# Kernel optimization log

Hardware: AMD Instinct MI355X
Metric: run time of the kernel (lower is better)

The kernel has to match this reference:

```python
import jax, jax.numpy as jnp
import numpy as np

B, S, D_MODEL, HEADS, DK = 2, 2048, 1024, 16, 64


def setup_inputs() -> dict:
    key = jax.random.key(0)
    ks = jax.random.split(key, 7)
    scale = 0.02
    return {
        "query": jax.random.normal(ks[0], (B, S, D_MODEL), jnp.float32),
        "key": jax.random.normal(ks[1], (B, S, D_MODEL), jnp.float32),
        "value": jax.random.normal(ks[2], (B, S, D_MODEL), jnp.float32),
        "Wq": jax.random.normal(ks[3], (D_MODEL, HEADS * DK), jnp.float32) * scale,
        "bq": jax.random.normal(ks[4], (HEADS * DK,), jnp.float32) * scale,
        "Wo": jax.random.normal(ks[5], (HEADS * DK, D_MODEL), jnp.float32) * scale,
        "bo": jax.random.normal(ks[6], (D_MODEL,), jnp.float32) * scale,
    }


def reference(query, key, value, Wq, bq, Wo, bo):
    # NOTE: faithful to the original code, which (buggily) uses _W_q to
    # project query, key AND value, and scales by sqrt(seq_len), not sqrt(d_k).
    seq_len = key.shape[1]

    def split_heads(x):
        # [B,S,H*DK] -> [H,B,S,DK]; torch chunk(dim=-1)+cat(dim=0) stacks head h
        # (slice h*DK:(h+1)*DK) at batch block h.
        p = x @ Wq + bq
        b, s, _ = p.shape
        return p.reshape(b, s, HEADS, DK).transpose(2, 0, 1, 3)

    q = split_heads(query)   # [H,B,S,DK]
    k = split_heads(key)
    v = split_heads(value)

    inv_scale = jnp.float32(1.0 / np.sqrt(seq_len))
    scores = jnp.einsum("hbqd,hbkd->hbqk", q, k) * inv_scale  # [H,B,S,S]
    attn = jax.nn.softmax(scores, axis=-1)
    out = jnp.einsum("hbqk,hbkd->hbqd", attn, v)  # [H,B,S,DK]
    # inverse of chunk(dim=0)+cat(dim=-1): [H,B,S,DK] -> [B,S,H*DK]
    out = out.transpose(1, 2, 0, 3).reshape(query.shape[0], query.shape[1], HEADS * DK)
    return out @ Wo + bo
```

## Files before the change

kernel.cpp:

```cpp
#include <hip/hip_runtime.h>

#define DEVI __device__ __forceinline__

typedef short short4_t __attribute__((ext_vector_type(4)));
typedef short short8_t __attribute__((ext_vector_type(8)));
typedef __bf16 bf16x8 __attribute__((ext_vector_type(8)));
typedef float f32x4 __attribute__((ext_vector_type(4)));

DEVI short f2bf(float f) {
    union { float f; unsigned u; } v; v.f = f;
    unsigned r = (v.u + 0x7fffu + ((v.u >> 16) & 1u)) >> 16;
    return (short)r;
}

DEVI unsigned pack_ru(float a, float b) {
    union { float f; unsigned u; } x, y; x.f = a; y.f = b;
    return __builtin_amdgcn_perm(y.u + 0x8000u, x.u + 0x8000u, 0x07060302u);
}

DEVI void g2lds16(const short* g, short* l) {
    __builtin_amdgcn_global_load_lds(
        (const __attribute__((address_space(1))) void*)g,
        (__attribute__((address_space(3))) void*)l, 16, 0, 0);
}

__global__ __launch_bounds__(256) void prep_kernel(const float* __restrict__ q,
                                                   const float* __restrict__ k,
                                                   const float* __restrict__ v,
                                                   short* __restrict__ X,
                                                   const float* __restrict__ Wq,
                                                   short* __restrict__ WqT,
                                                   const float* __restrict__ Wo,
                                                   short* __restrict__ WoT) {
    __shared__ short T[64][65];
    const int bx = blockIdx.x;
    const int t = threadIdx.x;
    if (bx < 12288) {
        const size_t N1 = (size_t)4096 * 1024;
        size_t e = ((size_t)bx * 256 + t) * 4;
        const float* src; size_t off;
        if (e < N1)            { src = q; off = e; }
        else if (e < 2 * N1)   { src = k; off = e - N1; }
        else                   { src = v; off = e - 2 * N1; }
        f32x4 f = *(const f32x4*)(src + off);
        short4_t o;
        o[0] = f2bf(f[0]); o[1] = f2bf(f[1]); o[2] = f2bf(f[2]); o[3] = f2bf(f[3]);
        *(short4_t*)(X + e) = o;
        return;
    }
    const int which = bx - 12288;
    const float* W = (which < 256) ? Wq : Wo;
    short* Wt      = (which < 256) ? WqT : WoT;
    const int bxx = which & 255;
    const int kt = (bxx & 15) * 64, nt = (bxx >> 4) * 64;
#pragma unroll
    for (int r = 0; r < 4; ++r) {
        int kl = (t >> 4) + 16 * r;
        int n0 = (t & 15) * 4;
        f32x4 f = *(const f32x4*)(W + (size_t)(kt + kl) * 1024 + nt + n0);
#pragma unroll
        for (int j = 0; j < 4; ++j) T[n0 + j][kl] = f2bf(f[j]);
    }
    __syncthreads();
#pragma unroll
    for (int r = 0; r < 2; ++r) {
        int nl = (t >> 3) + 32 * r;
        int k0 = (t & 7) * 8;
        short8_t vv;
#pragma unroll
        for (int j = 0; j < 8; ++j) vv[j] = T[nl][k0 + j];
        *(short8_t*)(Wt + (size_t)(nt + nl) * 1024 + kt + k0) = vv;
    }
}

template <typename OutT>
__global__ __launch_bounds__(256) void gemm_bt_kernel(const short* __restrict__ A,
                                                      const short* __restrict__ Bt,
                                                      const float* __restrict__ bias,
                                                      OutT* __restrict__ C,
                                                      int M, int N, int K,
                                                      int qrows, float qscale) {
    __shared__ __align__(16) short As[2][128 * 32];
    __shared__ __align__(16) short Bs[2][128 * 32];
    const int tid  = threadIdx.x;
    const int lane = tid & 63, wave = tid >> 6;
    const int quad = lane >> 4, l16 = lane & 15;
    const int row0 = blockIdx.x * 128, col0 = blockIdx.y * 128;
    const int wm = (wave >> 1) * 64, wn = (wave & 1) * 64;
    const int srow = lane >> 2;
    const int scol = (lane & 3) * 8;
    f32x4 acc[4][4] = {};
#pragma unroll
    for (int r = 0; r < 2; ++r) {
        int rb = r * 64 + wave * 16;
        g2lds16(A  + (size_t)(row0 + rb + srow) * K + scol, &As[0][rb * 32]);
        g2lds16(Bt + (size_t)(col0 + rb + srow) * K + scol, &Bs[0][rb * 32]);
    }
    __syncthreads();
    int buf = 0;
    for (int k0 = 0; k0 < K; k0 += 32) {
        if (k0 + 32 < K) {
#pragma unroll
            for (int r = 0; r < 2; ++r) {
                int rb = r * 64 + wave * 16;
                g2lds16(A  + (size_t)(row0 + rb + srow) * K + k0 + 32 + scol, &As[buf ^ 1][rb * 32]);
                g2lds16(Bt + (size_t)(col0 + rb + srow) * K + k0 + 32 + scol, &Bs[buf ^ 1][rb * 32]);
            }
        }
        bf16x8 af[4], bfr[4];
#pragma unroll
        for (int mi = 0; mi < 4; ++mi) af[mi]  = *(const bf16x8*)&As[buf][(wm + mi * 16 + l16) * 32 + quad * 8];
#pragma unroll
        for (int ni = 0; ni < 4; ++ni) bfr[ni] = *(const bf16x8*)&Bs[buf][(wn + ni * 16 + l16) * 32 + quad * 8];
#pragma unroll
        for (int mi = 0; mi < 4; ++mi)
#pragma unroll
            for (int ni = 0; ni < 4; ++ni)
                acc[mi][ni] = __builtin_amdgcn_mfma_f32_16x16x32_bf16(af[mi], bfr[ni], acc[mi][ni], 0, 0, 0);
        __syncthreads();
        buf ^= 1;
    }
#pragma unroll
    for (int mi = 0; mi < 4; ++mi) {
#pragma unroll
        for (int ni = 0; ni < 4; ++ni) {
            int col = col0 + wn + ni * 16 + l16;
            float bv = bias[col];
#pragma unroll
            for (int i = 0; i < 4; ++i) {
                int row = row0 + wm + mi * 16 + quad * 4 + i;
                float val = acc[mi][ni][i] + bv;
                if (row < qrows) val *= qscale;
                if constexpr (sizeof(OutT) == 2) C[(size_t)row * N + col] = (OutT)f2bf(val);
                else                             C[(size_t)row * N + col] = (OutT)val;
            }
        }
    }
}

__global__ __launch_bounds__(256) void gemm_bt64_kernel(const short* __restrict__ A,
                                                        const short* __restrict__ Bt,
                                                        const float* __restrict__ bias,
                                                        float* __restrict__ C,
                                                        int M, int N, int K) {
    __shared__ __align__(16) short As[2][64 * 32];
    __shared__ __align__(16) short Bs[2][128 * 32];
    const int tid  = threadIdx.x;
    const int lane = tid & 63, wave = tid >> 6;
    const int quad = lane >> 4, l16 = lane & 15;
    const int row0 = blockIdx.x * 64, col0 = blockIdx.y * 128;
    const int wn = wave * 32;
    const int srow = lane >> 2;
    const int scol = (lane & 3) * 8;
    f32x4 acc[4][2] = {};
    {
        int rb = wave * 16;
        g2lds16(A + (size_t)(row0 + rb + srow) * K + scol, &As[0][rb * 32]);
#pragma unroll
        for (int r = 0; r < 2; ++r) {
            int rb2 = r * 64 + wave * 16;
            g2lds16(Bt + (size_t)(col0 + rb2 + srow) * K + scol, &Bs[0][rb2 * 32]);
        }
    }
    __syncthreads();
    int buf = 0;
    for (int k0 = 0; k0 < K; k0 += 32) {
        if (k0 + 32 < K) {
            int rb = wave * 16;
            g2lds16(A + (size_t)(row0 + rb + srow) * K + k0 + 32 + scol, &As[buf ^ 1][rb * 32]);
#pragma unroll
            for (int r = 0; r < 2; ++r) {
                int rb2 = r * 64 + wave * 16;
                g2lds16(Bt + (size_t)(col0 + rb2 + srow) * K + k0 + 32 + scol, &Bs[buf ^ 1][rb2 * 32]);
            }
        }
        bf16x8 af[4], bfr[2];
#pragma unroll
        for (int mi = 0; mi < 4; ++mi) af[mi]  = *(const bf16x8*)&As[buf][(mi * 16 + l16) * 32 + quad * 8];
#pragma unroll
        for (int ni = 0; ni < 2; ++ni) bfr[ni] = *(const bf16x8*)&Bs[buf][(wn + ni * 16 + l16) * 32 + quad * 8];
#pragma unroll
        for (int mi = 0; mi < 4; ++mi)
#pragma unroll
            for (int ni = 0; ni < 2; ++ni)
                acc[mi][ni] = __builtin_amdgcn_mfma_f32_16x16x32_bf16(af[mi], bfr[ni], acc[mi][ni], 0, 0, 0);
        __syncthreads();
        buf ^= 1;
    }
#pragma unroll
    for (int mi = 0; mi < 4; ++mi) {
#pragma unroll
        for (int ni = 0; ni < 2; ++ni) {
            int col = col0 + wn + ni * 16 + l16;
            float bv = bias[col];
#pragma unroll
            for (int i = 0; i < 4; ++i) {
                int row = row0 + mi * 16 + quad * 4 + i;
                C[(size_t)row * N + col] = acc[mi][ni][i] + bv;
            }
        }
    }
}

__global__ __launch_bounds__(256) void transpose_v_kernel(const short* __restrict__ Pv,
                                                          short* __restrict__ VT) {
    __shared__ short T[64][65];
    const int t = threadIdx.x;
    const int hb = blockIdx.x, st = blockIdx.y * 64;
    const int h = hb >> 1, b = hb & 1;
#pragma unroll
    for (int r = 0; r < 2; ++r) {
        int sl = (t >> 3) + 32 * r;
        short8_t v = *(const short8_t*)(Pv + (size_t)(b * 2048 + st + sl) * 1024 + h * 64 + (t & 7) * 8);
#pragma unroll
        for (int j = 0; j < 8; ++j) T[(t & 7) * 8 + j][sl] = v[j];
    }
    __syncthreads();
#pragma unroll
    for (int r = 0; r < 2; ++r) {
        int dl = (t >> 3) + 32 * r;
        short8_t v;
#pragma unroll
        for (int j = 0; j < 8; ++j) v[j] = T[dl][(t & 7) * 8 + j];
        *(short8_t*)(VT + ((size_t)hb * 64 + dl) * 2048 + st + (t & 7) * 8) = v;
    }
}

__global__ __launch_bounds__(256, 2) void attn_kernel(const short* __restrict__ P,
                                                      const short* __restrict__ VT,
                                                      short* __restrict__ O) {
    constexpr int LDK = 72;
    constexpr int LDV = 136;
    constexpr int LDO = 72;
    union SmemU {
        struct { short Ks[2][128 * LDK]; short Vs[2][64 * LDV]; } s;
        short OT[128 * LDO];
    };
    __shared__ __align__(16) SmemU sm;

    const int t = threadIdx.x;
    const int lane = t & 63, wave = t >> 6;
    const int quad = lane >> 4, l16 = lane & 15;
    const int bx = blockIdx.x;
    const int xcd = bx & 7, bi = bx >> 3;
    const int hb = xcd * 4 + (bi & 3), qt = bi >> 2;
    const int h = hb >> 1, b = hb & 1;
    const short* Pq  = P + (size_t)(b * 2048 + qt * 128) * 1024 + h * 64;
    const short* Pk  = P + (size_t)(4096 + b * 2048) * 1024 + h * 64;
    const short* VTh = VT + (size_t)hb * 64 * 2048;
    const int wq = wave * 32;

    bf16x8 qf[2][2];
#pragma unroll
    for (int miq = 0; miq < 2; ++miq)
#pragma unroll
        for (int kh = 0; kh < 2; ++kh)
            qf[miq][kh] = *(const bf16x8*)(Pq + (size_t)(wq + miq * 16 + l16) * 1024 + kh * 32 + quad * 8);

    bf16x8 ones;
#pragma unroll
    for (int j = 0; j < 8; ++j) ones[j] = (__bf16)1.0f;

    f32x4 oacc[4][2] = {};
    f32x4 osum[2] = {};

    const int krow = t >> 3, kc8 = (t & 7) * 8;
    const int kj = krow & 7, kq = krow >> 3;
    const int lrow32 = (kj >= 4 ? 16 + (kj - 4) : kj) + kq * 4;
    const int vrow = t >> 4, vc8 = (t & 15) * 8;

    short8_t kreg[4], vreg[4];
#pragma unroll
    for (int it = 0; it < 4; ++it) {
        kreg[it] = *(const short8_t*)(Pk + (size_t)(it * 32 + krow) * 1024 + kc8);
        vreg[it] = *(const short8_t*)(VTh + (size_t)(it * 16 + vrow) * 2048 + vc8);
    }

    for (int tile = 0; tile < 16; ++tile) {
        const int buf = tile & 1;
        short* Ksb = sm.s.Ks[buf];
        short* Vsb = sm.s.Vs[buf];
#pragma unroll
        for (int it = 0; it < 4; ++it) {
            *(short8_t*)&Ksb[(it * 32 + lrow32) * LDK + kc8] = kreg[it];
            *(short8_t*)&Vsb[(it * 16 + vrow) * LDV + vc8] = vreg[it];
        }
        __syncthreads();
        if (tile + 1 < 16) {
            int kv0 = (tile + 1) * 128;
#pragma unroll
            for (int it = 0; it < 4; ++it) {
                kreg[it] = *(const short8_t*)(Pk + (size_t)(kv0 + it * 32 + krow) * 1024 + kc8);
                vreg[it] = *(const short8_t*)(VTh + (size_t)(it * 16 + vrow) * 2048 + kv0 + vc8);
            }
        }
#pragma unroll
        for (int p = 0; p < 4; ++p) {
            bf16x8 aA0 = *(const bf16x8*)&Ksb[(p * 32 + l16) * LDK + quad * 8];
            bf16x8 aA1 = *(const bf16x8*)&Ksb[(p * 32 + l16) * LDK + 32 + quad * 8];
            bf16x8 aB0 = *(const bf16x8*)&Ksb[(p * 32 + 16 + l16) * LDK + quad * 8];
            bf16x8 aB1 = *(const bf16x8*)&Ksb[(p * 32 + 16 + l16) * LDK + 32 + quad * 8];
            bf16x8 vA[4];
#pragma unroll
            for (int di = 0; di < 4; ++di)
                vA[di] = *(const bf16x8*)&Vsb[(di * 16 + l16) * LDV + p * 32 + quad * 8];
            __builtin_amdgcn_s_setprio(1);
#pragma unroll
            for (int miq = 0; miq < 2; ++miq) {
                f32x4 sA = {}, sB = {};
                sA = __builtin_amdgcn_mfma_f32_16x16x32_bf16(aA0, qf[miq][0], sA, 0, 0, 0);
                sB = __builtin_amdgcn_mfma_f32_16x16x32_bf16(aB0, qf[miq][0], sB, 0, 0, 0);
                sA = __builtin_amdgcn_mfma_f32_16x16x32_bf16(aA1, qf[miq][1], sA, 0, 0, 0);
                sB = __builtin_amdgcn_mfma_f32_16x16x32_bf16(aB1, qf[miq][1], sB, 0, 0, 0);
                float eA0 = __builtin_amdgcn_exp2f(sA[0]);
                float eA1 = __builtin_amdgcn_exp2f(sA[1]);
                float eA2 = __builtin_amdgcn_exp2f(sA[2]);
                float eA3 = __builtin_amdgcn_exp2f(sA[3]);
                float eB0 = __builtin_amdgcn_exp2f(sB[0]);
                float eB1 = __builtin_amdgcn_exp2f(sB[1]);
                float eB2 = __builtin_amdgcn_exp2f(sB[2]);
                float eB3 = __builtin_amdgcn_exp2f(sB[3]);
                union { unsigned u[4]; bf16x8 b8; } pb;
                pb.u[0] = pack_ru(eA0, eA1);
                pb.u[1] = pack_ru(eA2, eA3);
                pb.u[2] = pack_ru(eB0, eB1);
                pb.u[3] = pack_ru(eB2, eB3);
                osum[miq] = __builtin_amdgcn_mfma_f32_16x16x32_bf16(ones, pb.b8, osum[miq], 0, 0, 0);
#pragma unroll
                for (int di = 0; di < 4; ++di)
                    oacc[di][miq] = __builtin_amdgcn_mfma_f32_16x16x32_bf16(vA[di], pb.b8, oacc[di][miq], 0, 0, 0);
            }
            __builtin_amdgcn_s_setprio(0);
        }
    }

    float rinv[2];
#pragma unroll
    for (int miq = 0; miq < 2; ++miq) rinv[miq] = 1.0f / osum[miq][0];

    __syncthreads();

#pragma unroll
    for (int di = 0; di < 4; ++di) {
#pragma unroll
        for (int miq = 0; miq < 2; ++miq) {
            float v0 = oacc[di][miq][0] * rinv[miq];
            float v1 = oacc[di][miq][1] * rinv[miq];
            float v2 = oacc[di][miq][2] * rinv[miq];
            float v3 = oacc[di][miq][3] * rinv[miq];
            uint2 w;
            w.x = pack_ru(v0, v1);
            w.y = pack_ru(v2, v3);
            int q = wq + miq * 16 + l16;
            *(uint2*)&sm.OT[q * LDO + di * 16 + quad * 4] = w;
        }
    }
    __syncthreads();
    {
        const int orow = t >> 1, ocol = (t & 1) * 32;
        short* dst = O + (size_t)(b * 2048 + qt * 128 + orow) * 1024 + h * 64 + ocol;
#pragma unroll
        for (int c = 0; c < 4; ++c)
            *(short8_t*)(dst + c * 8) = *(const short8_t*)&sm.OT[orow * LDO + ocol + c * 8];
    }
}

extern "C" void kernel_launch(void* const* d_in, const int* in_sizes, int n_in,
                              void* d_out, int out_size, void* d_ws, size_t ws_size,
                              hipStream_t stream) {
    (void)in_sizes; (void)n_in; (void)out_size; (void)ws_size;
    const float* q  = (const float*)d_in[0];
    const float* k  = (const float*)d_in[1];
    const float* v  = (const float*)d_in[2];
    const float* Wq = (const float*)d_in[3];
    const float* bq = (const float*)d_in[4];
    const float* Wo = (const float*)d_in[5];
    const float* bo = (const float*)d_in[6];
    float* out = (float*)d_out;

    short* Xcat = (short*)d_ws;
    short* WqT  = Xcat + (size_t)12288 * 1024;
    short* WoT  = WqT + (size_t)1024 * 1024;
    short* P    = WoT + (size_t)1024 * 1024;
    short* VT   = P + (size_t)12288 * 1024;
    short* O    = VT + (size_t)32 * 64 * 2048;

    const float qscale = 0.022097086912079608f * 1.4426950408889634f;

    prep_kernel<<<12800, 256, 0, stream>>>(q, k, v, Xcat, Wq, WqT, Wo, WoT);
    gemm_bt_kernel<short><<<dim3(96, 8), 256, 0, stream>>>(Xcat, WqT, bq, P, 12288, 1024, 1024, 4096, qscale);
    transpose_v_kernel<<<dim3(32, 32), 256, 0, stream>>>(P + (size_t)8192 * 1024, VT);
    attn_kernel<<<512, 256, 0, stream>>>(P, VT, O);
    gemm_bt64_kernel<<<dim3(64, 8), 256, 0, stream>>>(O, WoT, bo, out, 4096, 1024, 1024);
}
```

Measured before the change: 205.6 us.

## Triple-buffer GEMM LDS staging with partial vmcnt waits and raw barriers

Both bf16 GEMM kernels move from double-buffered to triple-buffered LDS tiles, prefetching two K-steps ahead. A custom barrier waits only until the oldest stage's global-to-LDS loads have landed (vmcnt(N)), so one stage stays in flight across each barrier. The aim is to hide global load latency better than the old full-drain __syncthreads. In exchange, LDS use per block grows by half, which may reduce occupancy, and the hand-written waitcnt counts must exactly match the number of loads issued per stage.

```diff
diff --git a/kernel.cpp b/kernel.cpp
--- a/kernel.cpp
+++ b/kernel.cpp
@@ -23,6 +23,13 @@
         (const __attribute__((address_space(1))) void*)g,
         (__attribute__((address_space(3))) void*)l, 16, 0, 0);
 }
+
+#define CBAR(N)  do {                                          \
+    asm volatile("s_waitcnt vmcnt(" #N ")" ::: "memory");      \
+    __builtin_amdgcn_sched_barrier(0);                         \
+    __builtin_amdgcn_s_barrier();                              \
+    __builtin_amdgcn_sched_barrier(0);                         \
+} while (0)
 
 __global__ __launch_bounds__(256) void prep_kernel(const float* __restrict__ q,
                                                    const float* __restrict__ k,
@@ -80,8 +87,8 @@
                                                       OutT* __restrict__ C,
                                                       int M, int N, int K,
                                                       int qrows, float qscale) {
-    __shared__ __align__(16) short As[2][128 * 32];
-    __shared__ __align__(16) short Bs[2][128 * 32];
+    __shared__ __align__(16) short As[3][128 * 32];
+    __shared__ __align__(16) short Bs[3][128 * 32];
     const int tid  = threadIdx.x;
     const int lane = tid & 63, wave = tid >> 6;
     const int quad = lane >> 4, l16 = lane & 15;
@@ -90,23 +97,23 @@
     const int srow = lane >> 2;
     const int scol = (lane & 3) * 8;
     f32x4 acc[4][4] = {};
-#pragma unroll
-    for (int r = 0; r < 2; ++r) {
-        int rb = r * 64 + wave * 16;
-        g2lds16(A  + (size_t)(row0 + rb + srow) * K + scol, &As[0][rb * 32]);
-        g2lds16(Bt + (size_t)(col0 + rb + srow) * K + scol, &Bs[0][rb * 32]);
-    }
-    __syncthreads();
-    int buf = 0;
-    for (int k0 = 0; k0 < K; k0 += 32) {
-        if (k0 + 32 < K) {
-#pragma unroll
-            for (int r = 0; r < 2; ++r) {
-                int rb = r * 64 + wave * 16;
-                g2lds16(A  + (size_t)(row0 + rb + srow) * K + k0 + 32 + scol, &As[buf ^ 1][rb * 32]);
-                g2lds16(Bt + (size_t)(col0 + rb + srow) * K + k0 + 32 + scol, &Bs[buf ^ 1][rb * 32]);
-            }
-        }
+
+    const int nt = K >> 5;
+#define STAGE_BT(bi, k0) do {                                                        \
+        _Pragma("unroll")                                                            \
+        for (int r = 0; r < 2; ++r) {                                                \
+            int rb = r * 64 + wave * 16;                                             \
+            g2lds16(A  + (size_t)(row0 + rb + srow) * K + (k0) + scol, &As[bi][rb * 32]); \
+            g2lds16(Bt + (size_t)(col0 + rb + srow) * K + (k0) + scol, &Bs[bi][rb * 32]); \
+        }                                                                            \
+    } while (0)
+
+    STAGE_BT(0, 0);
+    STAGE_BT(1, 32);
+    CBAR(4);
+    for (int t = 0; t < nt; ++t) {
+        const int buf = t % 3;
+        if (t + 2 < nt) STAGE_BT((t + 2) % 3, (t + 2) * 32);
         bf16x8 af[4], bfr[4];
 #pragma unroll
         for (int mi = 0; mi < 4; ++mi) af[mi]  = *(const bf16x8*)&As[buf][(wm + mi * 16 + l16) * 32 + quad * 8];
@@ -117,9 +124,12 @@
 #pragma unroll
             for (int ni = 0; ni < 4; ++ni)
                 acc[mi][ni] = __builtin_amdgcn_mfma_f32_16x16x32_bf16(af[mi], bfr[ni], acc[mi][ni], 0, 0, 0);
-        __syncthreads();
-        buf ^= 1;
-    }
+        if (t + 1 < nt) {
+            if (t + 2 < nt) { CBAR(4); }
+            else            { CBAR(0); }
+        }
+    }
+#undef STAGE_BT
 #pragma unroll
     for (int mi = 0; mi < 4; ++mi) {
 #pragma unroll
@@ -143,8 +153,8 @@
                                                         const float* __restrict__ bias,
                                                         float* __restrict__ C,
                                                         int M, int N, int K) {
-    __shared__ __align__(16) short As[2][64 * 32];
-    __shared__ __align__(16) short Bs[2][128 * 32];
+    __shared__ __align__(16) short As[3][64 * 32];
+    __shared__ __align__(16) short Bs[3][128 * 32];
     const int tid  = threadIdx.x;
     const int lane = tid & 63, wave = tid >> 6;
     const int quad = lane >> 4, l16 = lane & 15;
@@ -153,27 +163,24 @@
     const int srow = lane >> 2;
     const int scol = (lane & 3) * 8;
     f32x4 acc[4][2] = {};
-    {
-        int rb = wave * 16;
-        g2lds16(A + (size_t)(row0 + rb + srow) * K + scol, &As[0][rb * 32]);
-#pragma unroll
-        for (int r = 0; r < 2; ++r) {
-            int rb2 = r * 64 + wave * 16;
-            g2lds16(Bt + (size_t)(col0 + rb2 + srow) * K + scol, &Bs[0][rb2 * 32]);
-        }
-    }
-    __syncthreads();
-    int buf = 0;
-    for (int k0 = 0; k0 < K; k0 += 32) {
-        if (k0 + 32 < K) {
-            int rb = wave * 16;
-            g2lds16(A + (size_t)(row0 + rb + srow) * K + k0 + 32 + scol, &As[buf ^ 1][rb * 32]);
-#pragma unroll
-            for (int r = 0; r < 2; ++r) {
-                int rb2 = r * 64 + wave * 16;
-                g2lds16(Bt + (size_t)(col0 + rb2 + srow) * K + k0 + 32 + scol, &Bs[buf ^ 1][rb2 * 32]);
-            }
-        }
+
+    const int nt = K >> 5;
+#define STAGE_B64(bi, k0) do {                                                       \
+        int rb = wave * 16;                                                          \
+        g2lds16(A + (size_t)(row0 + rb + srow) * K + (k0) + scol, &As[bi][rb * 32]); \
+        _Pragma("unroll")                                                            \
+        for (int r = 0; r < 2; ++r) {                                                \
+            int rb2 = r * 64 + wave * 16;                                            \
+            g2lds16(Bt + (size_t)(col0 + rb2 + srow) * K + (k0) + scol, &Bs[bi][rb2 * 32]); \
+        }                                                                            \
+    } while (0)
+
+    STAGE_B64(0, 0);
+    STAGE_B64(1, 32);
+    CBAR(3);
+    for (int t = 0; t < nt; ++t) {
+        const int buf = t % 3;
+        if (t + 2 < nt) STAGE_B64((t + 2) % 3, (t + 2) * 32);
         bf16x8 af[4], bfr[2];
 #pragma unroll
         for (int mi = 0; mi < 4; ++mi) af[mi]  = *(const bf16x8*)&As[buf][(mi * 16 + l16) * 32 + quad * 8];
@@ -184,9 +191,12 @@
 #pragma unroll
             for (int ni = 0; ni < 2; ++ni)
                 acc[mi][ni] = __builtin_amdgcn_mfma_f32_16x16x32_bf16(af[mi], bfr[ni], acc[mi][ni], 0, 0, 0);
-        __syncthreads();
-        buf ^= 1;
-    }
+        if (t + 1 < nt) {
+            if (t + 2 < nt) { CBAR(3); }
+            else            { CBAR(0); }
+        }
+    }
+#undef STAGE_B64
 #pragma unroll
     for (int mi = 0; mi < 4; ++mi) {
 #pragma unroll
```

Result: slower. 211.8 us (+3.0%).

## Fuse fp32-to-bf16 conversion of activations into the QKV projection GEMM

Applied to the files above, without the earlier changes.

Drops the separate pass that converts query/key/value from fp32 to bf16 into a workspace buffer. The QKV GEMM now loads fp32 A tiles straight into registers, converts them in-kernel and writes them to LDS, overlapping that with the MFMA loop. This removes a full write and re-read of a 24MB intermediate. In exchange, each GEMM tile reads twice the bytes for A (reused across 8 column blocks), uses more registers, and rounding changes from round-to-nearest-even to round-half-up.

```diff
diff --git a/kernel.cpp b/kernel.cpp
--- a/kernel.cpp
+++ b/kernel.cpp
@@ -24,31 +24,13 @@
         (__attribute__((address_space(3))) void*)l, 16, 0, 0);
 }
 
-__global__ __launch_bounds__(256) void prep_kernel(const float* __restrict__ q,
-                                                   const float* __restrict__ k,
-                                                   const float* __restrict__ v,
-                                                   short* __restrict__ X,
-                                                   const float* __restrict__ Wq,
-                                                   short* __restrict__ WqT,
-                                                   const float* __restrict__ Wo,
-                                                   short* __restrict__ WoT) {
+__global__ __launch_bounds__(256) void prepw_kernel(const float* __restrict__ Wq,
+                                                    short* __restrict__ WqT,
+                                                    const float* __restrict__ Wo,
+                                                    short* __restrict__ WoT) {
     __shared__ short T[64][65];
-    const int bx = blockIdx.x;
+    const int which = blockIdx.x;
     const int t = threadIdx.x;
-    if (bx < 12288) {
-        const size_t N1 = (size_t)4096 * 1024;
-        size_t e = ((size_t)bx * 256 + t) * 4;
-        const float* src; size_t off;
-        if (e < N1)            { src = q; off = e; }
-        else if (e < 2 * N1)   { src = k; off = e - N1; }
-        else                   { src = v; off = e - 2 * N1; }
-        f32x4 f = *(const f32x4*)(src + off);
-        short4_t o;
-        o[0] = f2bf(f[0]); o[1] = f2bf(f[1]); o[2] = f2bf(f[2]); o[3] = f2bf(f[3]);
-        *(short4_t*)(X + e) = o;
-        return;
-    }
-    const int which = bx - 12288;
     const float* W = (which < 256) ? Wq : Wo;
     short* Wt      = (which < 256) ? WqT : WoT;
     const int bxx = which & 255;
@@ -74,12 +56,14 @@
 }
 
 template <typename OutT>
-__global__ __launch_bounds__(256) void gemm_bt_kernel(const short* __restrict__ A,
-                                                      const short* __restrict__ Bt,
-                                                      const float* __restrict__ bias,
-                                                      OutT* __restrict__ C,
-                                                      int M, int N, int K,
-                                                      int qrows, float qscale) {
+__global__ __launch_bounds__(256) void gemm_qkv_kernel(const float* __restrict__ q,
+                                                       const float* __restrict__ kk,
+                                                       const float* __restrict__ v,
+                                                       const short* __restrict__ Bt,
+                                                       const float* __restrict__ bias,
+                                                       OutT* __restrict__ C,
+                                                       float qscale) {
+    constexpr int K = 1024, N = 1024;
     __shared__ __align__(16) short As[2][128 * 32];
     __shared__ __align__(16) short Bs[2][128 * 32];
     const int tid  = threadIdx.x;
@@ -89,23 +73,51 @@
     const int wm = (wave >> 1) * 64, wn = (wave & 1) * 64;
     const int srow = lane >> 2;
     const int scol = (lane & 3) * 8;
+    const float* Af = (row0 < 4096) ? (q  + (size_t)row0 * K)
+                    : (row0 < 8192) ? (kk + (size_t)(row0 - 4096) * K)
+                                    : (v  + (size_t)(row0 - 8192) * K);
+    const float oscale = (row0 < 4096) ? qscale : 1.0f;
     f32x4 acc[4][4] = {};
-#pragma unroll
-    for (int r = 0; r < 2; ++r) {
-        int rb = r * 64 + wave * 16;
-        g2lds16(A  + (size_t)(row0 + rb + srow) * K + scol, &As[0][rb * 32]);
-        g2lds16(Bt + (size_t)(col0 + rb + srow) * K + scol, &Bs[0][rb * 32]);
-    }
+    f32x4 ar[2][2];
+
+#define LOADA(k0) do {                                                                  \
+        _Pragma("unroll")                                                               \
+        for (int r = 0; r < 2; ++r) {                                                   \
+            int row = r * 64 + wave * 16 + srow;                                        \
+            ar[r][0] = *(const f32x4*)(Af + (size_t)row * K + (k0) + scol);             \
+            ar[r][1] = *(const f32x4*)(Af + (size_t)row * K + (k0) + scol + 4);         \
+        }                                                                               \
+    } while (0)
+#define STAGEB(bi, k0) do {                                                             \
+        _Pragma("unroll")                                                               \
+        for (int r = 0; r < 2; ++r) {                                                   \
+            int rb = r * 64 + wave * 16;                                                \
+            g2lds16(Bt + (size_t)(col0 + rb + srow) * K + (k0) + scol, &Bs[bi][rb * 32]); \
+        }                                                                               \
+    } while (0)
+#define WRITEA(bi) do {                                                                 \
+        _Pragma("unroll")                                                               \
+        for (int r = 0; r < 2; ++r) {                                                   \
+            int row = r * 64 + wave * 16 + srow;                                        \
+            union { unsigned u[4]; short8_t s8; } w;                                    \
+            w.u[0] = pack_ru(ar[r][0][0], ar[r][0][1]);                                 \
+            w.u[1] = pack_ru(ar[r][0][2], ar[r][0][3]);                                 \
+            w.u[2] = pack_ru(ar[r][1][0], ar[r][1][1]);                                 \
+            w.u[3] = pack_ru(ar[r][1][2], ar[r][1][3]);                                 \
+            *(short8_t*)&As[bi][row * 32 + scol] = w.s8;                                \
+        }                                                                               \
+    } while (0)
+
+    LOADA(0);
+    STAGEB(0, 0);
+    WRITEA(0);
     __syncthreads();
     int buf = 0;
     for (int k0 = 0; k0 < K; k0 += 32) {
-        if (k0 + 32 < K) {
-#pragma unroll
-            for (int r = 0; r < 2; ++r) {
-                int rb = r * 64 + wave * 16;
-                g2lds16(A  + (size_t)(row0 + rb + srow) * K + k0 + 32 + scol, &As[buf ^ 1][rb * 32]);
-                g2lds16(Bt + (size_t)(col0 + rb + srow) * K + k0 + 32 + scol, &Bs[buf ^ 1][rb * 32]);
-            }
+        const bool more = (k0 + 32 < K);
+        if (more) {
+            LOADA(k0 + 32);
+            STAGEB(buf ^ 1, k0 + 32);
         }
         bf16x8 af[4], bfr[4];
 #pragma unroll
@@ -117,9 +129,13 @@
 #pragma unroll
             for (int ni = 0; ni < 4; ++ni)
                 acc[mi][ni] = __builtin_amdgcn_mfma_f32_16x16x32_bf16(af[mi], bfr[ni], acc[mi][ni], 0, 0, 0);
+        if (more) WRITEA(buf ^ 1);
         __syncthreads();
         buf ^= 1;
     }
+#undef LOADA
+#undef STAGEB
+#undef WRITEA
 #pragma unroll
     for (int mi = 0; mi < 4; ++mi) {
 #pragma unroll
@@ -129,10 +145,8 @@
 #pragma unroll
             for (int i = 0; i < 4; ++i) {
                 int row = row0 + wm + mi * 16 + quad * 4 + i;
-                float val = acc[mi][ni][i] + bv;
-                if (row < qrows) val *= qscale;
-                if constexpr (sizeof(OutT) == 2) C[(size_t)row * N + col] = (OutT)f2bf(val);
-                else                             C[(size_t)row * N + col] = (OutT)val;
+                float val = (acc[mi][ni][i] + bv) * oscale;
+                C[(size_t)row * N + col] = (OutT)f2bf(val);
             }
         }
     }
@@ -378,17 +392,16 @@
     const float* bo = (const float*)d_in[6];
     float* out = (float*)d_out;
 
-    short* Xcat = (short*)d_ws;
-    short* WqT  = Xcat + (size_t)12288 * 1024;
-    short* WoT  = WqT + (size_t)1024 * 1024;
-    short* P    = WoT + (size_t)1024 * 1024;
-    short* VT   = P + (size_t)12288 * 1024;
-    short* O    = VT + (size_t)32 * 64 * 2048;
+    short* WqT = (short*)d_ws;
+    short* WoT = WqT + (size_t)1024 * 1024;
+    short* P   = WoT + (size_t)1024 * 1024;
+    short* VT  = P + (size_t)12288 * 1024;
+    short* O   = VT + (size_t)32 * 64 * 2048;
 
     const float qscale = 0.022097086912079608f * 1.4426950408889634f;
 
-    prep_kernel<<<12800, 256, 0, stream>>>(q, k, v, Xcat, Wq, WqT, Wo, WoT);
-    gemm_bt_kernel<short><<<dim3(96, 8), 256, 0, stream>>>(Xcat, WqT, bq, P, 12288, 1024, 1024, 4096, qscale);
+    prepw_kernel<<<512, 256, 0, stream>>>(Wq, WqT, Wo, WoT);
+    gemm_qkv_kernel<short><<<dim3(96, 8), 256, 0, stream>>>(q, k, v, WqT, bq, P, qscale);
     transpose_v_kernel<<<dim3(32, 32), 256, 0, stream>>>(P + (size_t)8192 * 1024, VT);
     attn_kernel<<<512, 256, 0, stream>>>(P, VT, O);
     gemm_bt64_kernel<<<dim3(64, 8), 256, 0, stream>>>(O, WoT, bo, out, 4096, 1024, 1024);
```

Result: no change. 206.0 us (+0.2%).
